# Kernel optimization log

Measured on AMD Instinct MI355X. Metric: run time of the kernel, lower is better.

## Reference

```python
import jax, jax.numpy as jnp
import numpy as np

N = 16384   # num_nodes (also in_channels: identity-style features)
C = 256     # hidden channels
K = 16      # num_classes
E = 524288  # num edges


def gcn_conv(x, src, dst, ew, W, b, num_nodes):
    """PyG GCNConv: linear transform, then sym-normalized scatter-add aggregation.
    Self-loops (weight 1) are appended; norm = d^-1/2[src] * w * d^-1/2[dst]."""
    h = x @ W                                            # [N, out]
    loop = jnp.arange(num_nodes, dtype=src.dtype)
    s = jnp.concatenate([src, loop])
    d = jnp.concatenate([dst, loop])
    w = jnp.concatenate([ew, jnp.ones((num_nodes,), ew.dtype)])
    deg = jax.ops.segment_sum(w, d, num_segments=num_nodes)
    dinv = jnp.where(deg > 0, jax.lax.rsqrt(jnp.maximum(deg, 1e-12)), 0.0)
    norm = dinv[s] * w * dinv[d]                         # [E+N]
    msg = norm[:, None] * h[s]                           # gather + scale
    out = jax.ops.segment_sum(msg, d, num_segments=num_nodes)  # scatter-add
    return out + b


def setup_inputs() -> dict:
    key = jax.random.key(0)
    k1, k2, k3, k4, k5, k6, k7 = jax.random.split(key, 7)
    x = jax.random.normal(k1, (N, N), dtype=jnp.float32)
    edge_index = jax.random.randint(k2, (2, E), 0, N, dtype=jnp.int64)
    edge_weight = jax.random.uniform(k3, (E,), dtype=jnp.float32)
    # GCNConv parameters (glorot-ish scale)
    W1 = jax.random.normal(k4, (N, C), dtype=jnp.float32) / np.sqrt(N)
    b1 = jnp.zeros((C,), jnp.float32)
    W2 = jax.random.normal(k5, (C, K), dtype=jnp.float32) / np.sqrt(C)
    b2 = jnp.zeros((K,), jnp.float32)
    return {"x": x, "edge_index": edge_index, "edge_weight": edge_weight,
            "W1": W1, "b1": b1, "W2": W2, "b2": b2}


def reference(x, edge_index, edge_weight, W1, b1, W2, b2):
    src, dst = edge_index[0], edge_index[1]
    h = gcn_conv(x, src, dst, edge_weight, W1, b1, N)
    h = jax.nn.relu(h)
    # dropout p=0.5 is identity in eval mode (self.training == False)
    out = gcn_conv(h, src, dst, edge_weight, W2, b2, N)
    return out
```

## Files before the change

### kernel.cpp

```cpp
#include <hip/hip_runtime.h>
#include <stdint.h>


namespace {
constexpr int NN = 16384;
constexpr int CH = 256;
constexpr int KC = 16;
constexpr int NE = 524288;
constexpr int KD = 16384;
constexpr int KSPLIT = 2;

constexpr size_t OFF_W1T  = 0;
constexpr size_t OFF_HP   = 8388608;
constexpr size_t OFF_HB   = 41943040;
constexpr size_t OFF_OUT1 = 50331648;
constexpr size_t OFF_H2   = 67108864;
constexpr size_t OFF_DEG  = 71303168;
constexpr size_t OFF_CNT  = 71368704;
constexpr size_t OFF_DINV = 71434240;
constexpr size_t OFF_ROWP = 71499776;
constexpr size_t OFF_CUR  = 71630848;
constexpr size_t OFF_COLS = 71761920;
constexpr size_t OFF_NRM  = 73859072;
}

typedef __attribute__((ext_vector_type(8))) short bf16x8;
typedef __attribute__((ext_vector_type(4))) float f32x4;

__device__ __forceinline__ unsigned short f2bf(float f) {
  unsigned int u = __builtin_bit_cast(unsigned int, f);
  u += 0x7fffu + ((u >> 16) & 1u);
  return (unsigned short)(u >> 16);
}
__device__ __forceinline__ float bf2f(unsigned short v) {
  unsigned int u = ((unsigned int)v) << 16;
  return __builtin_bit_cast(float, u);
}

__global__ __launch_bounds__(256)
void k_w1t(const float* __restrict__ w1, unsigned short* __restrict__ w1t) {
  __shared__ float tile[64][65];
  const int t = threadIdx.x;
  const int kb = blockIdx.x * 64;
  const int nb = blockIdx.y * 64;
  const int r = t >> 6;
  const int c = t & 63;
#pragma unroll
  for (int i = 0; i < 16; ++i)
    tile[i * 4 + r][c] = w1[(size_t)(kb + i * 4 + r) * CH + nb + c];
  __syncthreads();
#pragma unroll
  for (int i = 0; i < 16; ++i)
    w1t[(size_t)(nb + i * 4 + r) * KD + kb + c] = f2bf(tile[c][i * 4 + r]);
}

__global__ __launch_bounds__(256)
void k_deg(const int* __restrict__ dst, const float* __restrict__ ew,
           float* __restrict__ deg, int* __restrict__ cnt) {
  const int e = blockIdx.x * 256 + threadIdx.x;
  const int d = dst[e];
  atomicAdd(&deg[d], ew[e]);
  atomicAdd(&cnt[d], 1);
}

__global__ __launch_bounds__(256)
void k_dinv(const float* __restrict__ deg, float* __restrict__ dinv) {
  const int i = blockIdx.x * 256 + threadIdx.x;
  dinv[i] = rsqrtf(deg[i] + 1.0f);
}

__global__ __launch_bounds__(256)
void k_scan(const int* __restrict__ cnt, int* __restrict__ rowp, int* __restrict__ curs) {
  __shared__ int ps[256];
  const int t = threadIdx.x;
  const int base = t * 64;
  int s = 0;
  for (int j = 0; j < 64; ++j) s += cnt[base + j];
  ps[t] = s;
  __syncthreads();
  int v = s;
  for (int off = 1; off < 256; off <<= 1) {
    int u = (t >= off) ? ps[t - off] : 0;
    __syncthreads();
    v += u;
    ps[t] = v;
    __syncthreads();
  }
  int run = v - s;
  for (int j = 0; j < 64; ++j) {
    int c = cnt[base + j];
    rowp[base + j] = run;
    curs[base + j] = run;
    run += c;
  }
  if (t == 255) rowp[NN] = run;
}

__global__ __launch_bounds__(256)
void k_fill(const int* __restrict__ src, const int* __restrict__ dst,
            const float* __restrict__ ew, const float* __restrict__ dinv,
            int* __restrict__ curs, int* __restrict__ cols, float* __restrict__ nrm) {
  const int e = blockIdx.x * 256 + threadIdx.x;
  const int s = src[e], d = dst[e];
  const int pos = atomicAdd(&curs[d], 1);
  cols[pos] = s;
  nrm[pos] = dinv[s] * ew[e] * dinv[d];
}

__global__ __launch_bounds__(256)
void k_gemm1(const float* __restrict__ x, const unsigned short* __restrict__ w1t,
             float* __restrict__ hp) {
  __shared__ __align__(16) unsigned short As[2][64 * 32];
  __shared__ __align__(16) unsigned short Bs[2][256 * 32];

  const int tid  = threadIdx.x;
  const int lane = tid & 63;
  const int wave = tid >> 6;
  const int bm0  = (blockIdx.x >> 1) * 64;
  const int kb   = blockIdx.x & 1;
  const int koff = kb * (KD / KSPLIT);
  const int wn0  = wave * 64;

  const int ar  = tid >> 2;
  const int kq  = tid & 3;
  const int acn = kq ^ ((ar >> 1) & 3);
  const int aoff = ar * 32 + acn * 8;

  const int fr = lane & 15, fg = lane >> 4;
  const int fch = fg ^ ((fr >> 1) & 3);
  const int fA = fr * 32 + fch * 8;
  const int fB = (wn0 + fr) * 32 + fch * 8;

  const float* xrow = x + (size_t)(bm0 + ar) * KD + koff + kq * 8;
  const unsigned short* brow = w1t + (size_t)ar * KD + koff + kq * 8;

  float4 a0v, a1v;
  bf16x8 bv0, bv1, bv2, bv3;
  f32x4 acc[4][4] = {};

  auto LOADG = [&](int t) {
    const float* ap = xrow + (size_t)t * 32;
    a0v = *reinterpret_cast<const float4*>(ap);
    a1v = *reinterpret_cast<const float4*>(ap + 4);
    const unsigned short* bp = brow + (size_t)t * 32;
    bv0 = *reinterpret_cast<const bf16x8*>(bp);
    bv1 = *reinterpret_cast<const bf16x8*>(bp + (size_t)64 * KD);
    bv2 = *reinterpret_cast<const bf16x8*>(bp + (size_t)128 * KD);
    bv3 = *reinterpret_cast<const bf16x8*>(bp + (size_t)192 * KD);
  };
  auto STORE = [&](int buf) {
    bf16x8 ap;
    ap[0] = (short)f2bf(a0v.x); ap[1] = (short)f2bf(a0v.y);
    ap[2] = (short)f2bf(a0v.z); ap[3] = (short)f2bf(a0v.w);
    ap[4] = (short)f2bf(a1v.x); ap[5] = (short)f2bf(a1v.y);
    ap[6] = (short)f2bf(a1v.z); ap[7] = (short)f2bf(a1v.w);
    *reinterpret_cast<bf16x8*>(&As[buf][aoff]) = ap;
    *reinterpret_cast<bf16x8*>(&Bs[buf][(0 * 64 + ar) * 32 + acn * 8]) = bv0;
    *reinterpret_cast<bf16x8*>(&Bs[buf][(1 * 64 + ar) * 32 + acn * 8]) = bv1;
    *reinterpret_cast<bf16x8*>(&Bs[buf][(2 * 64 + ar) * 32 + acn * 8]) = bv2;
    *reinterpret_cast<bf16x8*>(&Bs[buf][(3 * 64 + ar) * 32 + acn * 8]) = bv3;
  };

  constexpr int NT = KD / KSPLIT / 32;
  LOADG(0);
  STORE(0);
  __syncthreads();
  int cur = 0;

  for (int t = 0; t < NT; ++t) {
    if (t + 1 < NT) LOADG(t + 1);
    bf16x8 af[4], bfr[4];
#pragma unroll
    for (int mi = 0; mi < 4; ++mi)
      af[mi] = *reinterpret_cast<const bf16x8*>(&As[cur][fA + mi * 512]);
#pragma unroll
    for (int ni = 0; ni < 4; ++ni)
      bfr[ni] = *reinterpret_cast<const bf16x8*>(&Bs[cur][fB + ni * 512]);
#pragma unroll
    for (int mi = 0; mi < 4; ++mi)
#pragma unroll
      for (int ni = 0; ni < 4; ++ni)
        acc[mi][ni] = __builtin_amdgcn_mfma_f32_16x16x32_bf16(af[mi], bfr[ni], acc[mi][ni], 0, 0, 0);
    if (t + 1 < NT) {
      STORE(cur ^ 1);
      __syncthreads();
      cur ^= 1;
    }
  }

  float* hpo = hp + (size_t)kb * NN * CH;
#pragma unroll
  for (int mi = 0; mi < 4; ++mi)
#pragma unroll
    for (int ni = 0; ni < 4; ++ni)
#pragma unroll
      for (int r = 0; r < 4; ++r) {
        const int m = bm0 + mi * 16 + fg * 4 + r;
        const int n = wn0 + ni * 16 + fr;
        hpo[(size_t)m * CH + n] = acc[mi][ni][r];
      }
}

__global__ __launch_bounds__(256)
void k_hred(const float* __restrict__ hp, unsigned short* __restrict__ hb) {
  const size_t i = ((size_t)blockIdx.x * 256 + threadIdx.x) * 8;
  const float4 a0 = *reinterpret_cast<const float4*>(hp + i);
  const float4 a1 = *reinterpret_cast<const float4*>(hp + i + 4);
  const float4 b0 = *reinterpret_cast<const float4*>(hp + (size_t)NN * CH + i);
  const float4 b1 = *reinterpret_cast<const float4*>(hp + (size_t)NN * CH + i + 4);
  bf16x8 o;
  o[0] = (short)f2bf(a0.x + b0.x); o[1] = (short)f2bf(a0.y + b0.y);
  o[2] = (short)f2bf(a0.z + b0.z); o[3] = (short)f2bf(a0.w + b0.w);
  o[4] = (short)f2bf(a1.x + b1.x); o[5] = (short)f2bf(a1.y + b1.y);
  o[6] = (short)f2bf(a1.z + b1.z); o[7] = (short)f2bf(a1.w + b1.w);
  *reinterpret_cast<bf16x8*>(hb + i) = o;
}

__global__ __launch_bounds__(256)
void k_agg1(const unsigned short* __restrict__ hb, const int* __restrict__ rowp,
            const int* __restrict__ cols, const float* __restrict__ nrm,
            const float* __restrict__ dinv, const float* __restrict__ b1,
            float* __restrict__ out1) {
  const int i = blockIdx.x;
  const int c = threadIdx.x;
  const int beg = rowp[i], end = rowp[i + 1];
  const float di = dinv[i];
  float acc = di * di * bf2f(hb[(size_t)i * CH + c]);
  int e = beg;
  for (; e + 2 <= end; e += 2) {
    const int s0 = cols[e], s1 = cols[e + 1];
    const float n0 = nrm[e], n1 = nrm[e + 1];
    acc += n0 * bf2f(hb[(size_t)s0 * CH + c]);
    acc += n1 * bf2f(hb[(size_t)s1 * CH + c]);
  }
  if (e < end) acc += nrm[e] * bf2f(hb[(size_t)cols[e] * CH + c]);
  out1[(size_t)i * CH + c] = fmaxf(acc + b1[c], 0.0f);
}

__global__ __launch_bounds__(256)
void k_gemm2(const float* __restrict__ out1, const float* __restrict__ w2,
             float* __restrict__ h2) {
  __shared__ float xs[16][256];
  __shared__ float ws[256 * 16];
  const int t = threadIdx.x;
  const int n0 = blockIdx.x * 16;
#pragma unroll
  for (int i = 0; i < 16; ++i) ws[i * 256 + t] = w2[i * 256 + t];
#pragma unroll
  for (int i = 0; i < 16; ++i) xs[i][t] = out1[(size_t)(n0 + i) * CH + t];
  __syncthreads();
  const int node = t >> 4, k = t & 15;
  float acc = 0.f;
#pragma unroll 8
  for (int c = 0; c < 256; ++c) acc += xs[node][c] * ws[c * 16 + k];
  h2[(size_t)(n0 + node) * KC + k] = acc;
}

__global__ __launch_bounds__(256)
void k_agg2(const float* __restrict__ h2, const int* __restrict__ rowp,
            const int* __restrict__ cols, const float* __restrict__ nrm,
            const float* __restrict__ dinv, const float* __restrict__ b2,
            float* __restrict__ out) {
  const int i = blockIdx.x * 4 + (threadIdx.x >> 6);
  const int lane = threadIdx.x & 63;
  const int k = lane & 15, g = lane >> 4;
  const int beg = rowp[i], end = rowp[i + 1];
  float acc = 0.f;
  for (int e = beg + g; e < end; e += 4)
    acc += nrm[e] * h2[(size_t)cols[e] * KC + k];
  acc += __shfl_xor(acc, 16);
  acc += __shfl_xor(acc, 32);
  if (g == 0) {
    const float di = dinv[i];
    out[(size_t)i * KC + k] = acc + di * di * h2[(size_t)i * KC + k] + b2[k];
  }
}

extern "C" void kernel_launch(void* const* d_in, const int* in_sizes, int n_in,
                              void* d_out, int out_size, void* d_ws, size_t ws_size,
                              hipStream_t stream) {
  const float* x  = (const float*)d_in[0];
  const int*   ei = (const int*)d_in[1];
  const float* ew = (const float*)d_in[2];
  const float* w1 = (const float*)d_in[3];
  const float* b1 = (const float*)d_in[4];
  const float* w2 = (const float*)d_in[5];
  const float* b2 = (const float*)d_in[6];
  const int* src = ei;
  const int* dst = ei + NE;

  uint8_t* ws = (uint8_t*)d_ws;
  unsigned short* w1t = (unsigned short*)(ws + OFF_W1T);
  float* hp   = (float*)(ws + OFF_HP);
  unsigned short* hb = (unsigned short*)(ws + OFF_HB);
  float* out1 = (float*)(ws + OFF_OUT1);
  float* h2   = (float*)(ws + OFF_H2);
  float* deg  = (float*)(ws + OFF_DEG);
  int*   cnt  = (int*)(ws + OFF_CNT);
  float* dinv = (float*)(ws + OFF_DINV);
  int*   rowp = (int*)(ws + OFF_ROWP);
  int*   curs = (int*)(ws + OFF_CUR);
  int*   cols = (int*)(ws + OFF_COLS);
  float* nrm  = (float*)(ws + OFF_NRM);
  float* out  = (float*)d_out;

  hipMemsetAsync(ws + OFF_DEG, 0, 131072, stream);

  k_w1t <<<dim3(256, 4), 256, 0, stream>>>(w1, w1t);
  k_deg <<<NE / 256, 256, 0, stream>>>(dst, ew, deg, cnt);
  k_dinv<<<NN / 256, 256, 0, stream>>>(deg, dinv);
  k_scan<<<1, 256, 0, stream>>>(cnt, rowp, curs);
  k_fill<<<NE / 256, 256, 0, stream>>>(src, dst, ew, dinv, curs, cols, nrm);
  k_gemm1<<<(NN / 64) * KSPLIT, 256, 0, stream>>>(x, w1t, hp);
  k_hred<<<NN * CH / (256 * 8), 256, 0, stream>>>(hp, hb);
  k_agg1<<<NN, 256, 0, stream>>>(hb, rowp, cols, nrm, dinv, b1, out1);
  k_gemm2<<<NN / 16, 256, 0, stream>>>(out1, w2, h2);
  k_agg2<<<NN / 4, 256, 0, stream>>>(h2, rowp, cols, nrm, dinv, b2, out);
}
```

Baseline: 541.6 us.

## Enlarge GEMM1 M-tile, use direct global-to-LDS B loads, XCD-aware mapping

GEMM1 now computes 128-row tiles instead of 64, doubling per-block reuse of the W1 slice, and raises the K split from 2 to 4 so the grid keeps its 512-block count. Blocks are remapped so each XCD handles one K-partition, and the B operand is copied straight into LDS with global_load_lds using a swizzle that matches the reader. The partial-sum reduction is generalised to four partials, which adds extra fp32 traffic and workspace. Layer-1 aggregation stages neighbour indices and norms in LDS chunks instead of each thread reading them from global memory.

```diff
diff --git a/kernel.cpp b/kernel.cpp
--- a/kernel.cpp
+++ b/kernel.cpp
@@ -8,20 +8,21 @@
 constexpr int KC = 16;
 constexpr int NE = 524288;
 constexpr int KD = 16384;
-constexpr int KSPLIT = 2;
+constexpr int KSPLIT = 4;
+constexpr int BM = 128;
 
 constexpr size_t OFF_W1T  = 0;
 constexpr size_t OFF_HP   = 8388608;
-constexpr size_t OFF_HB   = 41943040;
-constexpr size_t OFF_OUT1 = 50331648;
-constexpr size_t OFF_H2   = 67108864;
-constexpr size_t OFF_DEG  = 71303168;
-constexpr size_t OFF_CNT  = 71368704;
-constexpr size_t OFF_DINV = 71434240;
-constexpr size_t OFF_ROWP = 71499776;
-constexpr size_t OFF_CUR  = 71630848;
-constexpr size_t OFF_COLS = 71761920;
-constexpr size_t OFF_NRM  = 73859072;
+constexpr size_t OFF_HB   = 75497472;
+constexpr size_t OFF_OUT1 = 83886080;
+constexpr size_t OFF_H2   = 100663296;
+constexpr size_t OFF_DEG  = 101711872;
+constexpr size_t OFF_CNT  = 101777408;
+constexpr size_t OFF_DINV = 101842944;
+constexpr size_t OFF_ROWP = 101908480;
+constexpr size_t OFF_CUR  = 102039552;
+constexpr size_t OFF_COLS = 102105088;
+constexpr size_t OFF_NRM  = 104202240;
 }
 
 typedef __attribute__((ext_vector_type(8))) short bf16x8;
@@ -110,79 +111,99 @@
 __global__ __launch_bounds__(256)
 void k_gemm1(const float* __restrict__ x, const unsigned short* __restrict__ w1t,
              float* __restrict__ hp) {
-  __shared__ __align__(16) unsigned short As[2][64 * 32];
+  __shared__ __align__(16) unsigned short As[2][BM * 32];
   __shared__ __align__(16) unsigned short Bs[2][256 * 32];
 
   const int tid  = threadIdx.x;
   const int lane = tid & 63;
   const int wave = tid >> 6;
-  const int bm0  = (blockIdx.x >> 1) * 64;
-  const int kb   = blockIdx.x & 1;
+
+  const int bid  = blockIdx.x;
+  const int xcd  = bid & 7;
+  const int slot = bid >> 3;
+  const int kb   = xcd >> 1;
+  const int bm0  = (slot * 2 + (xcd & 1)) * BM;
   const int koff = kb * (KD / KSPLIT);
   const int wn0  = wave * 64;
 
-  const int ar  = tid >> 2;
+  const int r0  = tid >> 2;
   const int kq  = tid & 3;
-  const int acn = kq ^ ((ar >> 1) & 3);
-  const int aoff = ar * 32 + acn * 8;
+  const int acn = kq ^ ((r0 >> 1) & 3);
+  const int aoff0 = r0 * 32 + acn * 8;
+  const int aoff1 = (r0 + 64) * 32 + acn * 8;
+
+  const int cc = (lane & 3) ^ ((lane >> 3) & 3);
+  const unsigned short* bbase =
+      w1t + (size_t)(wave * 64 + (lane >> 2)) * KD + koff + cc * 8;
 
   const int fr = lane & 15, fg = lane >> 4;
   const int fch = fg ^ ((fr >> 1) & 3);
   const int fA = fr * 32 + fch * 8;
   const int fB = (wn0 + fr) * 32 + fch * 8;
 
-  const float* xrow = x + (size_t)(bm0 + ar) * KD + koff + kq * 8;
-  const unsigned short* brow = w1t + (size_t)ar * KD + koff + kq * 8;
-
-  float4 a0v, a1v;
-  bf16x8 bv0, bv1, bv2, bv3;
-  f32x4 acc[4][4] = {};
-
-  auto LOADG = [&](int t) {
-    const float* ap = xrow + (size_t)t * 32;
-    a0v = *reinterpret_cast<const float4*>(ap);
-    a1v = *reinterpret_cast<const float4*>(ap + 4);
-    const unsigned short* bp = brow + (size_t)t * 32;
-    bv0 = *reinterpret_cast<const bf16x8*>(bp);
-    bv1 = *reinterpret_cast<const bf16x8*>(bp + (size_t)64 * KD);
-    bv2 = *reinterpret_cast<const bf16x8*>(bp + (size_t)128 * KD);
-    bv3 = *reinterpret_cast<const bf16x8*>(bp + (size_t)192 * KD);
+  const float* xrow0 = x + (size_t)(bm0 + r0) * KD + koff + kq * 8;
+  const float* xrow1 = xrow0 + (size_t)64 * KD;
+
+  float4 a00, a01, a10, a11;
+  f32x4 acc[8][4] = {};
+
+  auto GLOADB = [&](int t, int buf) {
+    const unsigned short* g = bbase + (size_t)t * 32;
+#pragma unroll
+    for (int i = 0; i < 4; ++i) {
+      __builtin_amdgcn_global_load_lds(
+          (const __attribute__((address_space(1))) void*)(g + (size_t)i * 16 * KD),
+          (__attribute__((address_space(3))) void*)(&Bs[buf][(wave * 64 + i * 16) * 32]),
+          16, 0, 0);
+    }
   };
-  auto STORE = [&](int buf) {
-    bf16x8 ap;
-    ap[0] = (short)f2bf(a0v.x); ap[1] = (short)f2bf(a0v.y);
-    ap[2] = (short)f2bf(a0v.z); ap[3] = (short)f2bf(a0v.w);
-    ap[4] = (short)f2bf(a1v.x); ap[5] = (short)f2bf(a1v.y);
-    ap[6] = (short)f2bf(a1v.z); ap[7] = (short)f2bf(a1v.w);
-    *reinterpret_cast<bf16x8*>(&As[buf][aoff]) = ap;
-    *reinterpret_cast<bf16x8*>(&Bs[buf][(0 * 64 + ar) * 32 + acn * 8]) = bv0;
-    *reinterpret_cast<bf16x8*>(&Bs[buf][(1 * 64 + ar) * 32 + acn * 8]) = bv1;
-    *reinterpret_cast<bf16x8*>(&Bs[buf][(2 * 64 + ar) * 32 + acn * 8]) = bv2;
-    *reinterpret_cast<bf16x8*>(&Bs[buf][(3 * 64 + ar) * 32 + acn * 8]) = bv3;
+  auto LOADA = [&](int t) {
+    const float* p0 = xrow0 + (size_t)t * 32;
+    const float* p1 = xrow1 + (size_t)t * 32;
+    a00 = *reinterpret_cast<const float4*>(p0);
+    a01 = *reinterpret_cast<const float4*>(p0 + 4);
+    a10 = *reinterpret_cast<const float4*>(p1);
+    a11 = *reinterpret_cast<const float4*>(p1 + 4);
   };
+  auto STOREA = [&](int buf) {
+    bf16x8 v;
+    v[0] = (short)f2bf(a00.x); v[1] = (short)f2bf(a00.y);
+    v[2] = (short)f2bf(a00.z); v[3] = (short)f2bf(a00.w);
+    v[4] = (short)f2bf(a01.x); v[5] = (short)f2bf(a01.y);
+    v[6] = (short)f2bf(a01.z); v[7] = (short)f2bf(a01.w);
+    *reinterpret_cast<bf16x8*>(&As[buf][aoff0]) = v;
+    v[0] = (short)f2bf(a10.x); v[1] = (short)f2bf(a10.y);
+    v[2] = (short)f2bf(a10.z); v[3] = (short)f2bf(a10.w);
+    v[4] = (short)f2bf(a11.x); v[5] = (short)f2bf(a11.y);
+    v[6] = (short)f2bf(a11.z); v[7] = (short)f2bf(a11.w);
+    *reinterpret_cast<bf16x8*>(&As[buf][aoff1]) = v;
+  };
 
   constexpr int NT = KD / KSPLIT / 32;
-  LOADG(0);
-  STORE(0);
+  GLOADB(0, 0);
+  LOADA(0);
+  STOREA(0);
   __syncthreads();
   int cur = 0;
 
   for (int t = 0; t < NT; ++t) {
-    if (t + 1 < NT) LOADG(t + 1);
-    bf16x8 af[4], bfr[4];
-#pragma unroll
-    for (int mi = 0; mi < 4; ++mi)
-      af[mi] = *reinterpret_cast<const bf16x8*>(&As[cur][fA + mi * 512]);
+    if (t + 1 < NT) {
+      GLOADB(t + 1, cur ^ 1);
+      LOADA(t + 1);
+    }
+    bf16x8 bfr[4];
 #pragma unroll
     for (int ni = 0; ni < 4; ++ni)
       bfr[ni] = *reinterpret_cast<const bf16x8*>(&Bs[cur][fB + ni * 512]);
 #pragma unroll
-    for (int mi = 0; mi < 4; ++mi)
+    for (int mi = 0; mi < 8; ++mi) {
+      const bf16x8 af = *reinterpret_cast<const bf16x8*>(&As[cur][fA + mi * 512]);
 #pragma unroll
       for (int ni = 0; ni < 4; ++ni)
-        acc[mi][ni] = __builtin_amdgcn_mfma_f32_16x16x32_bf16(af[mi], bfr[ni], acc[mi][ni], 0, 0, 0);
+        acc[mi][ni] = __builtin_amdgcn_mfma_f32_16x16x32_bf16(af, bfr[ni], acc[mi][ni], 0, 0, 0);
+    }
     if (t + 1 < NT) {
-      STORE(cur ^ 1);
+      STOREA(cur ^ 1);
       __syncthreads();
       cur ^= 1;
     }
@@ -190,7 +211,7 @@
 
   float* hpo = hp + (size_t)kb * NN * CH;
 #pragma unroll
-  for (int mi = 0; mi < 4; ++mi)
+  for (int mi = 0; mi < 8; ++mi)
 #pragma unroll
     for (int ni = 0; ni < 4; ++ni)
 #pragma unroll
@@ -204,15 +225,20 @@
 __global__ __launch_bounds__(256)
 void k_hred(const float* __restrict__ hp, unsigned short* __restrict__ hb) {
   const size_t i = ((size_t)blockIdx.x * 256 + threadIdx.x) * 8;
-  const float4 a0 = *reinterpret_cast<const float4*>(hp + i);
-  const float4 a1 = *reinterpret_cast<const float4*>(hp + i + 4);
-  const float4 b0 = *reinterpret_cast<const float4*>(hp + (size_t)NN * CH + i);
-  const float4 b1 = *reinterpret_cast<const float4*>(hp + (size_t)NN * CH + i + 4);
+  float s[8];
+#pragma unroll
+  for (int j = 0; j < 8; ++j) s[j] = 0.f;
+#pragma unroll
+  for (int p = 0; p < KSPLIT; ++p) {
+    const float* q = hp + (size_t)p * NN * CH + i;
+    const float4 v0 = *reinterpret_cast<const float4*>(q);
+    const float4 v1 = *reinterpret_cast<const float4*>(q + 4);
+    s[0] += v0.x; s[1] += v0.y; s[2] += v0.z; s[3] += v0.w;
+    s[4] += v1.x; s[5] += v1.y; s[6] += v1.z; s[7] += v1.w;
+  }
   bf16x8 o;
-  o[0] = (short)f2bf(a0.x + b0.x); o[1] = (short)f2bf(a0.y + b0.y);
-  o[2] = (short)f2bf(a0.z + b0.z); o[3] = (short)f2bf(a0.w + b0.w);
-  o[4] = (short)f2bf(a1.x + b1.x); o[5] = (short)f2bf(a1.y + b1.y);
-  o[6] = (short)f2bf(a1.z + b1.z); o[7] = (short)f2bf(a1.w + b1.w);
+#pragma unroll
+  for (int j = 0; j < 8; ++j) o[j] = (short)f2bf(s[j]);
   *reinterpret_cast<bf16x8*>(hb + i) = o;
 }
 
@@ -221,19 +247,21 @@
             const int* __restrict__ cols, const float* __restrict__ nrm,
             const float* __restrict__ dinv, const float* __restrict__ b1,
             float* __restrict__ out1) {
+  __shared__ int   scols[64];
+  __shared__ float snrm[64];
   const int i = blockIdx.x;
   const int c = threadIdx.x;
   const int beg = rowp[i], end = rowp[i + 1];
   const float di = dinv[i];
   float acc = di * di * bf2f(hb[(size_t)i * CH + c]);
-  int e = beg;
-  for (; e + 2 <= end; e += 2) {
-    const int s0 = cols[e], s1 = cols[e + 1];
-    const float n0 = nrm[e], n1 = nrm[e + 1];
-    acc += n0 * bf2f(hb[(size_t)s0 * CH + c]);
-    acc += n1 * bf2f(hb[(size_t)s1 * CH + c]);
-  }
-  if (e < end) acc += nrm[e] * bf2f(hb[(size_t)cols[e] * CH + c]);
+  for (int base = beg; base < end; base += 64) {
+    const int m = min(64, end - base);
+    __syncthreads();
+    if (c < m) { scols[c] = cols[base + c]; snrm[c] = nrm[base + c]; }
+    __syncthreads();
+    for (int j = 0; j < m; ++j)
+      acc += snrm[j] * bf2f(hb[(size_t)scols[j] * CH + c]);
+  }
   out1[(size_t)i * CH + c] = fmaxf(acc + b1[c], 0.0f);
 }
 
@@ -311,7 +339,7 @@
   k_dinv<<<NN / 256, 256, 0, stream>>>(deg, dinv);
   k_scan<<<1, 256, 0, stream>>>(cnt, rowp, curs);
   k_fill<<<NE / 256, 256, 0, stream>>>(src, dst, ew, dinv, curs, cols, nrm);
-  k_gemm1<<<(NN / 64) * KSPLIT, 256, 0, stream>>>(x, w1t, hp);
+  k_gemm1<<<(NN / BM) * KSPLIT, 256, 0, stream>>>(x, w1t, hp);
   k_hred<<<NN * CH / (256 * 8), 256, 0, stream>>>(hp, hb);
   k_agg1<<<NN, 256, 0, stream>>>(hb, rowp, cols, nrm, dinv, b1, out1);
   k_gemm2<<<NN / 16, 256, 0, stream>>>(out1, w2, h2);
```

New measurement: 484.3 us. -10.6%, faster.
